# Kernel tuning notes

Hardware: AMD Instinct MI355X
Metric: run time of the kernel (lower is better)

## Reference

```python
import jax, jax.numpy as jnp
import numpy as np


def setup_inputs() -> dict:
    key = jax.random.key(0)
    k1, k2 = jax.random.split(key)
    B, C, H, W = 8, 19, 512, 512
    pred = jax.random.normal(k1, (B, C, H, W), dtype=jnp.float32)
    target = jax.random.randint(k2, (B, H, W), 0, C)
    return {"pred": pred, "target": target}


def reference(pred, target):
    B, C, H, W = pred.shape
    N = H * W
    p = jax.nn.softmax(pred, axis=1).reshape(B, C, N)                      # [B,C,N]
    # one-hot float target per class: target_flat = (target == c).float()
    tgt = (target.reshape(B, 1, N) == jnp.arange(C)[None, :, None]).astype(p.dtype)  # [B,C,N]
    signs = 2.0 * tgt - 1.0
    errors = 1.0 - p * signs                                               # [B,C,N]
    # descending sort of errors; permutation applied to the target too
    perm = jnp.argsort(-errors, axis=-1)                                   # [B,C,N]
    errors_sorted = jnp.take_along_axis(errors, perm, axis=-1)
    gt_sorted = jnp.take_along_axis(tgt, perm, axis=-1)
    # Lovasz gradient (Jaccard extension gradient)
    gts = jnp.sum(gt_sorted, axis=-1, keepdims=True)                       # [B,C,1]
    intersection = gts - jnp.cumsum(gt_sorted, axis=-1)
    union = gts + jnp.cumsum(1.0 - gt_sorted, axis=-1)
    jaccard = 1.0 - intersection / union
    grad = jnp.concatenate([jaccard[..., :1], jaccard[..., 1:] - jaccard[..., :-1]], axis=-1)
    # dot(relu(errors_sorted), grad) per (b,c), then mean over B*C
    loss_bc = jnp.sum(jax.nn.relu(errors_sorted) * grad, axis=-1)          # [B,C]
    return jnp.sum(loss_bc) / (B * C)
```

## Files before the change

### kernel.cpp

```cpp
#include <hip/hip_runtime.h>

#define BATCH 8
#define NCLS  19
#define LOGN  18
#define NPIX  (1u << LOGN)
#define NB    64
#define BLK1  512
#define BPB   64
#define HCOPY 8
#define HSTR  (NCLS * NB + 4)

__global__ __launch_bounds__(BLK1, 4) void k_hist(
    const float* __restrict__ pred, const int* __restrict__ target,
    unsigned short* __restrict__ hist_part, float* __restrict__ s2_part)
{
    __shared__ unsigned hist[HCOPY * HSTR];
    __shared__ float    s2w[BLK1 / 64][NCLS];

    const int b     = blockIdx.x / BPB;
    const int chunk = blockIdx.x % BPB;
    const int tid   = threadIdx.x;
    const int lane  = tid & 63;
    const int wid   = tid >> 6;

    unsigned* hpar = hist + (lane & (HCOPY - 1)) * HSTR;

    for (int i = tid; i < HCOPY * HSTR; i += BLK1) hist[i] = 0u;
    __syncthreads();

    float ps[NCLS];
    #pragma unroll
    for (int c = 0; c < NCLS; ++c) ps[c] = 0.0f;

    const float* pb   = pred + (((size_t)b * NCLS) << LOGN);
    const int*   tb   = target + ((size_t)b << LOGN);
    const int    base = chunk * (int)(NPIX / BPB);

    #pragma unroll 1
    for (int it = 0; it < (int)(NPIX / BPB) / (2 * BLK1); ++it) {
        const int n = base + it * (2 * BLK1) + 2 * tid;

        const int2 tg = *reinterpret_cast<const int2*>(tb + n);

        float2 e2[NCLS];
        float sA = 0.0f, sB = 0.0f;
        #pragma unroll
        for (int c = 0; c < NCLS; ++c) {
            const float2 x = *reinterpret_cast<const float2*>(pb + (((size_t)c) << LOGN) + n);
            const float eA = __expf(x.x);
            const float eB = __expf(x.y);
            e2[c].x = eA; e2[c].y = eB;
            sA += eA; sB += eB;
        }
        const float rA = __builtin_amdgcn_rcpf(sA) * (float)NB;
        const float rB = __builtin_amdgcn_rcpf(sB) * (float)NB;

        #pragma unroll
        for (int c = 0; c < NCLS; ++c) {
            const float tA = e2[c].x * rA;
            const float tB = e2[c].y * rB;
            int binA = (int)tA; binA = binA > NB - 1 ? NB - 1 : binA;
            int binB = (int)tB; binB = binB > NB - 1 ? NB - 1 : binB;
            ps[c] += ((c == tg.x) ? fmaf(tA, -1.0f / (float)NB, 1.0f) : 0.0f)
                   + ((c == tg.y) ? fmaf(tB, -1.0f / (float)NB, 1.0f) : 0.0f);
            if (c != tg.x) atomicAdd(&hpar[c * NB + binA], 1u);
            if (c != tg.y) atomicAdd(&hpar[c * NB + binB], 1u);
        }
    }
    __syncthreads();

    #pragma unroll
    for (int c = 0; c < NCLS; ++c) {
        float v = ps[c];
        #pragma unroll
        for (int off = 32; off > 0; off >>= 1) v += __shfl_down(v, off, 64);
        if (lane == 0) s2w[wid][c] = v;
    }
    __syncthreads();

    for (int i = tid; i < NCLS * NB; i += BLK1) {
        const int c = i >> 6, bin = i & (NB - 1);
        unsigned v = 0;
        #pragma unroll
        for (int k = 0; k < HCOPY; ++k) v += hist[k * HSTR + i];
        hist_part[((size_t)(b * NCLS + c) * BPB + chunk) * NB + bin] = (unsigned short)v;
    }
    if (tid < NCLS) {
        float v = 0.0f;
        #pragma unroll
        for (int w = 0; w < BLK1 / 64; ++w) v += s2w[w][tid];
        s2_part[(size_t)(b * NCLS + tid) * BPB + chunk] = v;
    }
}

__global__ __launch_bounds__(256) void k_finish(
    const unsigned short* __restrict__ hist_part, const float* __restrict__ s2_part,
    float* __restrict__ loss_bc)
{
    __shared__ unsigned hsum[4][NB];

    const int bc   = blockIdx.x;
    const int tid  = threadIdx.x;
    const int lane = tid & 63;
    const int w    = tid >> 6;

    const unsigned short* hp = hist_part + (size_t)bc * BPB * NB;
    unsigned h = 0;
    #pragma unroll 1
    for (int k = 0; k < BPB / 4; ++k)
        h += hp[(size_t)(w * (BPB / 4) + k) * NB + lane];
    hsum[w][lane] = h;
    __syncthreads();

    if (w == 0) {
        const unsigned hb = hsum[0][lane] + hsum[1][lane] + hsum[2][lane] + hsum[3][lane];
        const unsigned hrev = __shfl(hb, 63 - lane, 64);
        unsigned sc = hrev;
        #pragma unroll
        for (int off = 1; off < 64; off <<= 1) {
            const unsigned v = __shfl_up(sc, off, 64);
            if (lane >= off) sc += v;
        }
        const unsigned M   = __shfl(sc, 63, 64);
        const float    ncf = (float)(NPIX - M);
        const unsigned Rh  = sc;
        const unsigned Rab = sc - hrev;

        const float gR  = (Rab > 0) ? (float)Rab / ((float)Rab + ncf) : 0.0f;
        const float gRh = (Rh  > 0) ? (float)Rh  / ((float)Rh  + ncf) : 0.0f;

        float red = gR + gRh;
        float s2  = s2_part[(size_t)bc * BPB + lane];
        #pragma unroll
        for (int off = 32; off > 0; off >>= 1) {
            red += __shfl_down(red, off, 64);
            s2  += __shfl_down(s2,  off, 64);
        }
        if (lane == 0) {
            const float Nf = (float)NPIX;
            loss_bc[bc] = (float)M / Nf + red * (0.5f / (float)NB) + s2 / Nf;
        }
    }
}

__global__ __launch_bounds__(256) void k_reduce(
    const float* __restrict__ loss_bc, float* __restrict__ out)
{
    __shared__ float r[256];
    const int tid = threadIdx.x;
    r[tid] = (tid < BATCH * NCLS) ? loss_bc[tid] : 0.0f;
    __syncthreads();
    for (int off = 128; off > 0; off >>= 1) {
        if (tid < off) r[tid] += r[tid + off];
        __syncthreads();
    }
    if (tid == 0) out[0] = r[0] * (1.0f / (float)(BATCH * NCLS));
}

extern "C" void kernel_launch(void* const* d_in, const int* in_sizes, int n_in,
                              void* d_out, int out_size, void* d_ws, size_t ws_size,
                              hipStream_t stream)
{
    const float* pred   = (const float*)d_in[0];
    const int*   target = (const int*)d_in[1];
    float*       out    = (float*)d_out;
    unsigned char* ws   = (unsigned char*)d_ws;

    unsigned short* hist_part = (unsigned short*)ws;
    float* s2_part = (float*)(ws + (size_t)BATCH * NCLS * BPB * NB * sizeof(unsigned short));
    float* loss_bc = (float*)((unsigned char*)s2_part + (size_t)BATCH * NCLS * BPB * sizeof(float));

    hipLaunchKernelGGL(k_hist,   dim3(BATCH * BPB),  dim3(BLK1), 0, stream,
                       pred, target, hist_part, s2_part);
    hipLaunchKernelGGL(k_finish, dim3(BATCH * NCLS), dim3(256),  0, stream,
                       hist_part, s2_part, loss_bc);
    hipLaunchKernelGGL(k_reduce, dim3(1),            dim3(256),  0, stream,
                       loss_bc, out);
}
```

Baseline: 43.71 us.

## Skip bin-zero histogram atomics, double-buffer loads, track target counts separately

The histogram kernel no longer issues LDS atomics for bin 0, which is the most populated bin for softmax probabilities over 19 classes. It recovers that bin by counting target pixels per class in LDS and deriving the total in the finish kernel. The 4-iteration pixel loop is fully unrolled with two register buffers so global loads for the next chunk are issued before the current one is processed. Per-class s2 sums move from per-thread registers plus a shuffle reduction to LDS atomics. The cost is higher register pressure from holding two buffers and extra LDS float atomics, which contend on only 19 addresses.

```diff
diff --git a/kernel.cpp b/kernel.cpp
--- a/kernel.cpp
+++ b/kernel.cpp
@@ -7,97 +7,113 @@
 #define NB    64
 #define BLK1  512
 #define BPB   64
+#define PPB   (NPIX / BPB)
 #define HCOPY 8
 #define HSTR  (NCLS * NB + 4)
 
+struct Buf {
+    float2 x[NCLS];
+    int2   tg;
+};
+
+__device__ __forceinline__ void load_buf(Buf& bf, const float* __restrict__ pb,
+                                         const int* __restrict__ tb, int n) {
+    bf.tg = *reinterpret_cast<const int2*>(tb + n);
+    #pragma unroll
+    for (int c = 0; c < NCLS; ++c)
+        bf.x[c] = *reinterpret_cast<const float2*>(pb + ((size_t)c << LOGN) + n);
+}
+
+__device__ __forceinline__ void process(const Buf& bf, unsigned* __restrict__ hpar,
+                                        float* __restrict__ s2lds,
+                                        unsigned* __restrict__ cntlds) {
+    float2 e2[NCLS];
+    float sA = 0.f, sB = 0.f;
+    #pragma unroll
+    for (int c = 0; c < NCLS; ++c) {
+        const float eA = __expf(bf.x[c].x);
+        const float eB = __expf(bf.x[c].y);
+        e2[c].x = eA; e2[c].y = eB;
+        sA += eA; sB += eB;
+    }
+    const float rA = __builtin_amdgcn_rcpf(sA) * (float)NB;
+    const float rB = __builtin_amdgcn_rcpf(sB) * (float)NB;
+    const int tgA = bf.tg.x, tgB = bf.tg.y;
+    float etA = 0.f, etB = 0.f;
+    #pragma unroll
+    for (int c = 0; c < NCLS; ++c) {
+        const float tA = e2[c].x * rA;
+        const float tB = e2[c].y * rB;
+        etA = (c == tgA) ? e2[c].x : etA;
+        etB = (c == tgB) ? e2[c].y : etB;
+        int binA = (int)tA; binA = binA > NB - 1 ? NB - 1 : binA;
+        int binB = (int)tB; binB = binB > NB - 1 ? NB - 1 : binB;
+        if (c != tgA && binA != 0) atomicAdd(&hpar[c * NB + binA], 1u);
+        if (c != tgB && binB != 0) atomicAdd(&hpar[c * NB + binB], 1u);
+    }
+    const float s2A = fmaf(etA * rA, -1.0f / (float)NB, 1.0f);
+    const float s2B = fmaf(etB * rB, -1.0f / (float)NB, 1.0f);
+    atomicAdd(&s2lds[tgA], s2A);
+    atomicAdd(&s2lds[tgB], s2B);
+    atomicAdd(&cntlds[tgA], 1u);
+    atomicAdd(&cntlds[tgB], 1u);
+}
+
 __global__ __launch_bounds__(BLK1, 4) void k_hist(
     const float* __restrict__ pred, const int* __restrict__ target,
-    unsigned short* __restrict__ hist_part, float* __restrict__ s2_part)
+    unsigned short* __restrict__ hist_part, float* __restrict__ s2_part,
+    unsigned short* __restrict__ cnt_part)
 {
     __shared__ unsigned hist[HCOPY * HSTR];
-    __shared__ float    s2w[BLK1 / 64][NCLS];
+    __shared__ float    s2lds[NCLS];
+    __shared__ unsigned cntlds[NCLS];
 
     const int b     = blockIdx.x / BPB;
     const int chunk = blockIdx.x % BPB;
     const int tid   = threadIdx.x;
     const int lane  = tid & 63;
-    const int wid   = tid >> 6;
 
     unsigned* hpar = hist + (lane & (HCOPY - 1)) * HSTR;
 
     for (int i = tid; i < HCOPY * HSTR; i += BLK1) hist[i] = 0u;
-    __syncthreads();
-
-    float ps[NCLS];
-    #pragma unroll
-    for (int c = 0; c < NCLS; ++c) ps[c] = 0.0f;
-
-    const float* pb   = pred + (((size_t)b * NCLS) << LOGN);
-    const int*   tb   = target + ((size_t)b << LOGN);
-    const int    base = chunk * (int)(NPIX / BPB);
-
-    #pragma unroll 1
-    for (int it = 0; it < (int)(NPIX / BPB) / (2 * BLK1); ++it) {
-        const int n = base + it * (2 * BLK1) + 2 * tid;
-
-        const int2 tg = *reinterpret_cast<const int2*>(tb + n);
-
-        float2 e2[NCLS];
-        float sA = 0.0f, sB = 0.0f;
-        #pragma unroll
-        for (int c = 0; c < NCLS; ++c) {
-            const float2 x = *reinterpret_cast<const float2*>(pb + (((size_t)c) << LOGN) + n);
-            const float eA = __expf(x.x);
-            const float eB = __expf(x.y);
-            e2[c].x = eA; e2[c].y = eB;
-            sA += eA; sB += eB;
-        }
-        const float rA = __builtin_amdgcn_rcpf(sA) * (float)NB;
-        const float rB = __builtin_amdgcn_rcpf(sB) * (float)NB;
-
-        #pragma unroll
-        for (int c = 0; c < NCLS; ++c) {
-            const float tA = e2[c].x * rA;
-            const float tB = e2[c].y * rB;
-            int binA = (int)tA; binA = binA > NB - 1 ? NB - 1 : binA;
-            int binB = (int)tB; binB = binB > NB - 1 ? NB - 1 : binB;
-            ps[c] += ((c == tg.x) ? fmaf(tA, -1.0f / (float)NB, 1.0f) : 0.0f)
-                   + ((c == tg.y) ? fmaf(tB, -1.0f / (float)NB, 1.0f) : 0.0f);
-            if (c != tg.x) atomicAdd(&hpar[c * NB + binA], 1u);
-            if (c != tg.y) atomicAdd(&hpar[c * NB + binB], 1u);
-        }
-    }
-    __syncthreads();
-
-    #pragma unroll
-    for (int c = 0; c < NCLS; ++c) {
-        float v = ps[c];
-        #pragma unroll
-        for (int off = 32; off > 0; off >>= 1) v += __shfl_down(v, off, 64);
-        if (lane == 0) s2w[wid][c] = v;
-    }
+    if (tid < NCLS) { s2lds[tid] = 0.f; cntlds[tid] = 0u; }
+    __syncthreads();
+
+    const float* pb = pred + (((size_t)b * NCLS) << LOGN);
+    const int*   tb = target + ((size_t)b << LOGN);
+    const int    base = chunk * PPB + 2 * tid;
+
+    Buf A, B;
+    load_buf(A, pb, tb, base);
+    load_buf(B, pb, tb, base + 2 * BLK1);
+    process(A, hpar, s2lds, cntlds);
+    load_buf(A, pb, tb, base + 4 * BLK1);
+    process(B, hpar, s2lds, cntlds);
+    load_buf(B, pb, tb, base + 6 * BLK1);
+    process(A, hpar, s2lds, cntlds);
+    process(B, hpar, s2lds, cntlds);
+
     __syncthreads();
 
     for (int i = tid; i < NCLS * NB; i += BLK1) {
+        unsigned v = 0;
+        #pragma unroll
+        for (int k = 0; k < HCOPY; ++k) v += hist[k * HSTR + i];
         const int c = i >> 6, bin = i & (NB - 1);
-        unsigned v = 0;
-        #pragma unroll
-        for (int k = 0; k < HCOPY; ++k) v += hist[k * HSTR + i];
         hist_part[((size_t)(b * NCLS + c) * BPB + chunk) * NB + bin] = (unsigned short)v;
     }
     if (tid < NCLS) {
-        float v = 0.0f;
-        #pragma unroll
-        for (int w = 0; w < BLK1 / 64; ++w) v += s2w[w][tid];
-        s2_part[(size_t)(b * NCLS + tid) * BPB + chunk] = v;
+        s2_part [(size_t)(b * NCLS + tid) * BPB + chunk] = s2lds[tid];
+        cnt_part[(size_t)(b * NCLS + tid) * BPB + chunk] = (unsigned short)cntlds[tid];
     }
 }
 
 __global__ __launch_bounds__(256) void k_finish(
     const unsigned short* __restrict__ hist_part, const float* __restrict__ s2_part,
-    float* __restrict__ loss_bc)
+    const unsigned short* __restrict__ cnt_part, float* __restrict__ loss_bc)
 {
     __shared__ unsigned hsum[4][NB];
+    __shared__ float s2tot, nctot;
 
     const int bc   = blockIdx.x;
     const int tid  = threadIdx.x;
@@ -110,6 +126,19 @@
     for (int k = 0; k < BPB / 4; ++k)
         h += hp[(size_t)(w * (BPB / 4) + k) * NB + lane];
     hsum[w][lane] = h;
+
+    if (w == 1) {
+        float v = s2_part[(size_t)bc * BPB + lane];
+        #pragma unroll
+        for (int off = 32; off > 0; off >>= 1) v += __shfl_down(v, off, 64);
+        if (lane == 0) s2tot = v;
+    }
+    if (w == 2) {
+        unsigned v = cnt_part[(size_t)bc * BPB + lane];
+        #pragma unroll
+        for (int off = 32; off > 0; off >>= 1) v += __shfl_down(v, off, 64);
+        if (lane == 0) nctot = (float)v;
+    }
     __syncthreads();
 
     if (w == 0) {
@@ -121,25 +150,19 @@
             const unsigned v = __shfl_up(sc, off, 64);
             if (lane >= off) sc += v;
         }
-        const unsigned M   = __shfl(sc, 63, 64);
-        const float    ncf = (float)(NPIX - M);
-        const unsigned Rh  = sc;
+        const float ncf = nctot;
+        const float Nf  = (float)NPIX;
+        const float Mf  = Nf - ncf;
         const unsigned Rab = sc - hrev;
-
-        const float gR  = (Rab > 0) ? (float)Rab / ((float)Rab + ncf) : 0.0f;
-        const float gRh = (Rh  > 0) ? (float)Rh  / ((float)Rh  + ncf) : 0.0f;
-
+        float fRh = (float)sc;
+        if (lane == 63) fRh = Mf;
+        const float gR  = (Rab > 0)   ? (float)Rab / ((float)Rab + ncf) : 0.0f;
+        const float gRh = (fRh > 0.f) ? fRh / (fRh + ncf) : 0.0f;
         float red = gR + gRh;
-        float s2  = s2_part[(size_t)bc * BPB + lane];
-        #pragma unroll
-        for (int off = 32; off > 0; off >>= 1) {
-            red += __shfl_down(red, off, 64);
-            s2  += __shfl_down(s2,  off, 64);
-        }
-        if (lane == 0) {
-            const float Nf = (float)NPIX;
-            loss_bc[bc] = (float)M / Nf + red * (0.5f / (float)NB) + s2 / Nf;
-        }
+        #pragma unroll
+        for (int off = 32; off > 0; off >>= 1) red += __shfl_down(red, off, 64);
+        if (lane == 0)
+            loss_bc[bc] = Mf / Nf + red * (0.5f / (float)NB) + s2tot / Nf;
     }
 }
 
@@ -167,13 +190,17 @@
     unsigned char* ws   = (unsigned char*)d_ws;
 
     unsigned short* hist_part = (unsigned short*)ws;
-    float* s2_part = (float*)(ws + (size_t)BATCH * NCLS * BPB * NB * sizeof(unsigned short));
-    float* loss_bc = (float*)((unsigned char*)s2_part + (size_t)BATCH * NCLS * BPB * sizeof(float));
+    size_t off = (size_t)BATCH * NCLS * BPB * NB * sizeof(unsigned short);
+    float* s2_part = (float*)(ws + off);
+    off += (size_t)BATCH * NCLS * BPB * sizeof(float);
+    unsigned short* cnt_part = (unsigned short*)(ws + off);
+    off += (size_t)BATCH * NCLS * BPB * sizeof(unsigned short);
+    float* loss_bc = (float*)(ws + off);
 
     hipLaunchKernelGGL(k_hist,   dim3(BATCH * BPB),  dim3(BLK1), 0, stream,
-                       pred, target, hist_part, s2_part);
+                       pred, target, hist_part, s2_part, cnt_part);
     hipLaunchKernelGGL(k_finish, dim3(BATCH * NCLS), dim3(256),  0, stream,
-                       hist_part, s2_part, loss_bc);
+                       hist_part, s2_part, cnt_part, loss_bc);
     hipLaunchKernelGGL(k_reduce, dim3(1),            dim3(256),  0, stream,
                        loss_bc, out);
 }
```

New measurement: 45.73 us. 1.05x slower.

## Double blocks per batch, raise occupancy, and make histogram atomics branchless

Applied to the files above, without the earlier changes.

Makes the blocks-per-batch count a template parameter and picks 128 when the workspace is large enough, doubling grid parallelism and raising the launch-bounds occupancy hint to 8 blocks per CU. The inner loop no longer uses per-class register accumulators plus a shuffle reduction. Instead each thread records the target-class exp and issues a shared-memory float atomic into per-wave slots. Histogram atomics become unconditional, with target-class hits sent to a trash bin to avoid divergence, and the softmax sum uses a balanced tree. The cost is more partial histograms for the finish kernel to reduce and extra atomic traffic to the trash bin.

```diff
diff --git a/kernel.cpp b/kernel.cpp
--- a/kernel.cpp
+++ b/kernel.cpp
@@ -6,98 +6,101 @@
 #define NPIX  (1u << LOGN)
 #define NB    64
 #define BLK1  512
-#define BPB   64
 #define HCOPY 8
 #define HSTR  (NCLS * NB + 4)
+#define TRASHW (HCOPY * HSTR)
 
-__global__ __launch_bounds__(BLK1, 4) void k_hist(
+template<int BPB>
+__global__ __launch_bounds__(BLK1, 8) void k_hist(
     const float* __restrict__ pred, const int* __restrict__ target,
     unsigned short* __restrict__ hist_part, float* __restrict__ s2_part)
 {
-    __shared__ unsigned hist[HCOPY * HSTR];
-    __shared__ float    s2w[BLK1 / 64][NCLS];
+    constexpr int PPB = (int)(NPIX / BPB);
+
+    __shared__ unsigned hist[HCOPY * HSTR + NB];
+    __shared__ float    s2l[BLK1 / 64][NCLS];
 
     const int b     = blockIdx.x / BPB;
     const int chunk = blockIdx.x % BPB;
     const int tid   = threadIdx.x;
     const int lane  = tid & 63;
     const int wid   = tid >> 6;
+    const unsigned hbase = (unsigned)(lane & (HCOPY - 1)) * HSTR;
 
-    unsigned* hpar = hist + (lane & (HCOPY - 1)) * HSTR;
-
-    for (int i = tid; i < HCOPY * HSTR; i += BLK1) hist[i] = 0u;
+    for (int i = tid; i < HCOPY * HSTR + NB; i += BLK1) hist[i] = 0u;
+    if (tid < (BLK1 / 64) * NCLS) (&s2l[0][0])[tid] = 0.f;
     __syncthreads();
-
-    float ps[NCLS];
-    #pragma unroll
-    for (int c = 0; c < NCLS; ++c) ps[c] = 0.0f;
 
     const float* pb   = pred + (((size_t)b * NCLS) << LOGN);
     const int*   tb   = target + ((size_t)b << LOGN);
-    const int    base = chunk * (int)(NPIX / BPB);
+    const int    base = chunk * PPB;
 
     #pragma unroll 1
-    for (int it = 0; it < (int)(NPIX / BPB) / (2 * BLK1); ++it) {
+    for (int it = 0; it < PPB / (2 * BLK1); ++it) {
         const int n = base + it * (2 * BLK1) + 2 * tid;
-
         const int2 tg = *reinterpret_cast<const int2*>(tb + n);
 
         float2 e2[NCLS];
-        float sA = 0.0f, sB = 0.0f;
         #pragma unroll
         for (int c = 0; c < NCLS; ++c) {
             const float2 x = *reinterpret_cast<const float2*>(pb + (((size_t)c) << LOGN) + n);
-            const float eA = __expf(x.x);
-            const float eB = __expf(x.y);
-            e2[c].x = eA; e2[c].y = eB;
-            sA += eA; sB += eB;
+            e2[c].x = __expf(x.x);
+            e2[c].y = __expf(x.y);
         }
+        const float sA =
+            (((e2[0].x + e2[1].x) + (e2[2].x + e2[3].x)) + ((e2[4].x + e2[5].x) + (e2[6].x + e2[7].x)))
+          + (((e2[8].x + e2[9].x) + (e2[10].x + e2[11].x)) + ((e2[12].x + e2[13].x) + (e2[14].x + e2[15].x)))
+          + ((e2[16].x + e2[17].x) + e2[18].x);
+        const float sB =
+            (((e2[0].y + e2[1].y) + (e2[2].y + e2[3].y)) + ((e2[4].y + e2[5].y) + (e2[6].y + e2[7].y)))
+          + (((e2[8].y + e2[9].y) + (e2[10].y + e2[11].y)) + ((e2[12].y + e2[13].y) + (e2[14].y + e2[15].y)))
+          + ((e2[16].y + e2[17].y) + e2[18].y);
+
         const float rA = __builtin_amdgcn_rcpf(sA) * (float)NB;
         const float rB = __builtin_amdgcn_rcpf(sB) * (float)NB;
 
+        float etA = 0.f, etB = 0.f;
         #pragma unroll
         for (int c = 0; c < NCLS; ++c) {
             const float tA = e2[c].x * rA;
             const float tB = e2[c].y * rB;
             int binA = (int)tA; binA = binA > NB - 1 ? NB - 1 : binA;
             int binB = (int)tB; binB = binB > NB - 1 ? NB - 1 : binB;
-            ps[c] += ((c == tg.x) ? fmaf(tA, -1.0f / (float)NB, 1.0f) : 0.0f)
-                   + ((c == tg.y) ? fmaf(tB, -1.0f / (float)NB, 1.0f) : 0.0f);
-            if (c != tg.x) atomicAdd(&hpar[c * NB + binA], 1u);
-            if (c != tg.y) atomicAdd(&hpar[c * NB + binB], 1u);
+            const bool iA = (c == tg.x), iB = (c == tg.y);
+            etA = iA ? e2[c].x : etA;
+            etB = iB ? e2[c].y : etB;
+            const unsigned wA = iA ? (unsigned)TRASHW : hbase + c * NB;
+            const unsigned wB = iB ? (unsigned)TRASHW : hbase + c * NB;
+            atomicAdd(&hist[wA + (unsigned)binA], 1u);
+            atomicAdd(&hist[wB + (unsigned)binB], 1u);
         }
-    }
-    __syncthreads();
-
-    #pragma unroll
-    for (int c = 0; c < NCLS; ++c) {
-        float v = ps[c];
-        #pragma unroll
-        for (int off = 32; off > 0; off >>= 1) v += __shfl_down(v, off, 64);
-        if (lane == 0) s2w[wid][c] = v;
+        atomicAdd(&s2l[wid][tg.x], fmaf(etA * rA, -1.0f / (float)NB, 1.0f));
+        atomicAdd(&s2l[wid][tg.y], fmaf(etB * rB, -1.0f / (float)NB, 1.0f));
     }
     __syncthreads();
 
     for (int i = tid; i < NCLS * NB; i += BLK1) {
-        const int c = i >> 6, bin = i & (NB - 1);
         unsigned v = 0;
         #pragma unroll
         for (int k = 0; k < HCOPY; ++k) v += hist[k * HSTR + i];
+        const int c = i >> 6, bin = i & (NB - 1);
         hist_part[((size_t)(b * NCLS + c) * BPB + chunk) * NB + bin] = (unsigned short)v;
     }
     if (tid < NCLS) {
-        float v = 0.0f;
+        float v = 0.f;
         #pragma unroll
-        for (int w = 0; w < BLK1 / 64; ++w) v += s2w[w][tid];
+        for (int w = 0; w < BLK1 / 64; ++w) v += s2l[w][tid];
         s2_part[(size_t)(b * NCLS + tid) * BPB + chunk] = v;
     }
 }
 
+template<int BPB>
 __global__ __launch_bounds__(256) void k_finish(
     const unsigned short* __restrict__ hist_part, const float* __restrict__ s2_part,
     float* __restrict__ loss_bc)
 {
     __shared__ unsigned hsum[4][NB];
+    __shared__ float s2tot;
 
     const int bc   = blockIdx.x;
     const int tid  = threadIdx.x;
@@ -110,6 +113,14 @@
     for (int k = 0; k < BPB / 4; ++k)
         h += hp[(size_t)(w * (BPB / 4) + k) * NB + lane];
     hsum[w][lane] = h;
+
+    if (w == 1) {
+        float v = 0.f;
+        for (int k = lane; k < BPB; k += 64) v += s2_part[(size_t)bc * BPB + k];
+        #pragma unroll
+        for (int off = 32; off > 0; off >>= 1) v += __shfl_down(v, off, 64);
+        if (lane == 0) s2tot = v;
+    }
     __syncthreads();
 
     if (w == 0) {
@@ -130,15 +141,11 @@
         const float gRh = (Rh  > 0) ? (float)Rh  / ((float)Rh  + ncf) : 0.0f;
 
         float red = gR + gRh;
-        float s2  = s2_part[(size_t)bc * BPB + lane];
         #pragma unroll
-        for (int off = 32; off > 0; off >>= 1) {
-            red += __shfl_down(red, off, 64);
-            s2  += __shfl_down(s2,  off, 64);
-        }
+        for (int off = 32; off > 0; off >>= 1) red += __shfl_down(red, off, 64);
         if (lane == 0) {
             const float Nf = (float)NPIX;
-            loss_bc[bc] = (float)M / Nf + red * (0.5f / (float)NB) + s2 / Nf;
+            loss_bc[bc] = (float)M / Nf + red * (0.5f / (float)NB) + s2tot / Nf;
         }
     }
 }
@@ -157,6 +164,22 @@
     if (tid == 0) out[0] = r[0] * (1.0f / (float)(BATCH * NCLS));
 }
 
+template<int BPB>
+static void launch_all(const float* pred, const int* target, unsigned char* ws,
+                       float* out, hipStream_t stream)
+{
+    unsigned short* hist_part = (unsigned short*)ws;
+    float* s2_part = (float*)(ws + (size_t)BATCH * NCLS * BPB * NB * sizeof(unsigned short));
+    float* loss_bc = (float*)((unsigned char*)s2_part + (size_t)BATCH * NCLS * BPB * sizeof(float));
+
+    hipLaunchKernelGGL(k_hist<BPB>,   dim3(BATCH * BPB),  dim3(BLK1), 0, stream,
+                       pred, target, hist_part, s2_part);
+    hipLaunchKernelGGL(k_finish<BPB>, dim3(BATCH * NCLS), dim3(256),  0, stream,
+                       hist_part, s2_part, loss_bc);
+    hipLaunchKernelGGL(k_reduce,      dim3(1),            dim3(256),  0, stream,
+                       loss_bc, out);
+}
+
 extern "C" void kernel_launch(void* const* d_in, const int* in_sizes, int n_in,
                               void* d_out, int out_size, void* d_ws, size_t ws_size,
                               hipStream_t stream)
@@ -166,14 +189,11 @@
     float*       out    = (float*)d_out;
     unsigned char* ws   = (unsigned char*)d_ws;
 
-    unsigned short* hist_part = (unsigned short*)ws;
-    float* s2_part = (float*)(ws + (size_t)BATCH * NCLS * BPB * NB * sizeof(unsigned short));
-    float* loss_bc = (float*)((unsigned char*)s2_part + (size_t)BATCH * NCLS * BPB * sizeof(float));
+    auto need = [](int bpb) {
+        return (size_t)BATCH * NCLS * bpb * (NB * sizeof(unsigned short) + sizeof(float))
+             + (size_t)BATCH * NCLS * sizeof(float);
+    };
 
-    hipLaunchKernelGGL(k_hist,   dim3(BATCH * BPB),  dim3(BLK1), 0, stream,
-                       pred, target, hist_part, s2_part);
-    hipLaunchKernelGGL(k_finish, dim3(BATCH * NCLS), dim3(256),  0, stream,
-                       hist_part, s2_part, loss_bc);
-    hipLaunchKernelGGL(k_reduce, dim3(1),            dim3(256),  0, stream,
-                       loss_bc, out);
+    if (ws_size >= need(128)) launch_all<128>(pred, target, ws, out, stream);
+    else                      launch_all<64>(pred, target, ws, out, stream);
 }
```

Measured after the change: 56.64 us. 1.3x slower.
